# Kernel tuning notes

Hardware: AMD Instinct MI355X
Metric: run time of the kernel (lower is better)

Reference implementation:

```python
import jax, jax.numpy as jnp
import numpy as np

# Dimensions
B = 256        # number of graphs
NPG = 128      # nodes per graph (max_nodes; uniform -> to_dense_batch == reshape)
H = 8          # num_heads
DH = 32        # head_dim
HID = H * DH   # hidden_dim = 256
E = 524288     # n_edges
NGT = 20       # num_gate_types
EF = 8         # edge_feat_dim


def setup_inputs() -> dict:
    key = jax.random.key(0)
    ks = jax.random.split(key, 20)
    n_nodes = B * NPG
    x = jax.random.normal(ks[0], (n_nodes, HID), jnp.float32)
    # edges stay within the source node's graph
    src = jax.random.randint(ks[1], (E,), 0, n_nodes, dtype=jnp.int32)
    dst = (src // NPG) * NPG + jax.random.randint(ks[2], (E,), 0, NPG, dtype=jnp.int32)
    edge_index = jnp.stack([src, dst])  # [2, E]
    edge_attr = jax.random.normal(ks[3], (E, EF), jnp.float32)
    edge_gate_type = jax.random.randint(ks[4], (E,), 0, NGT, dtype=jnp.int32)
    batch = (jnp.arange(n_nodes) // NPG).astype(jnp.int32)

    s = 1.0 / np.sqrt(HID)
    def lin(k, din, dout, scale):
        kw, kb = jax.random.split(k)
        return (jax.random.uniform(kw, (din, dout), jnp.float32, -scale, scale),
                jax.random.uniform(kb, (dout,), jnp.float32, -scale, scale))
    Wq, bq = lin(ks[5], HID, HID, s)
    Wk, bk = lin(ks[6], HID, HID, s)
    Wv, bv = lin(ks[7], HID, HID, s)
    Wo, bo = lin(ks[8], HID, HID, s)
    gate_table = jax.random.normal(ks[9], (NGT, H), jnp.float32)
    We, be = lin(ks[10], EF, H, 1.0 / np.sqrt(EF))
    return {"x": x, "edge_attr": edge_attr, "Wq": Wq, "bq": bq, "Wk": Wk, "bk": bk,
            "Wv": Wv, "bv": bv, "Wo": Wo, "bo": bo, "gate_table": gate_table,
            "We": We, "be": be, "edge_index": edge_index,
            "edge_gate_type": edge_gate_type, "batch": batch}


def _edge_bias(edge_index, edge_attr, edge_gate_type, batch, gate_table, We, be):
    src, dst = edge_index[0], edge_index[1]
    eb = batch[src]                       # edge -> graph id
    src_l = src - eb * NPG                # local node index within graph
    dst_l = dst - eb * NPG
    total = gate_table[edge_gate_type] + edge_attr @ We + be   # [E, H]
    bias = jnp.zeros((B, H, NPG, NPG), edge_attr.dtype)
    bias = bias.at[eb, :, src_l, dst_l].add(total)             # forward direction
    rev = jnp.where((src_l != dst_l)[:, None], total, 0.0)     # skip self-loops
    bias = bias.at[eb, :, dst_l, src_l].add(rev)               # reverse direction
    return bias


def reference(x, edge_attr, Wq, bq, Wk, bk, Wv, bv, Wo, bo, gate_table, We, be,
              edge_index, edge_gate_type, batch):
    scale = 1.0 / np.sqrt(DH)
    xd = x.reshape(B, NPG, HID)  # uniform graph sizes -> to_dense_batch is a reshape
    Q = (xd @ Wq + bq).reshape(B, NPG, H, DH).transpose(0, 2, 1, 3)  # [B,H,N,D]
    K = (xd @ Wk + bk).reshape(B, NPG, H, DH).transpose(0, 2, 1, 3)
    V = (xd @ Wv + bv).reshape(B, NPG, H, DH).transpose(0, 2, 1, 3)
    scores = jnp.einsum('bhqd,bhkd->bhqk', Q, K) * scale
    scores = scores + _edge_bias(edge_index, edge_attr, edge_gate_type, batch,
                                 gate_table, We, be)
    attn = jax.nn.softmax(scores, axis=-1)  # node_mask all-True (uniform sizes)
    out = jnp.einsum('bhqk,bhkd->bhqd', attn, V)
    out = out.transpose(0, 2, 1, 3).reshape(B * NPG, HID)
    return out @ Wo + bo
```

## Files before the change

### kernel.cpp

```cpp
#include <hip/hip_runtime.h>
#include <hip/hip_fp16.h>

typedef unsigned short u16;
typedef unsigned int u32;
typedef __attribute__((ext_vector_type(8))) short short8;
typedef __attribute__((ext_vector_type(4))) float f32x4;

#define MFMA16(a, b, c) __builtin_amdgcn_mfma_f32_16x16x32_bf16((a), (b), (c), 0, 0, 0)

#define ESTRIDE 2304

#define FIXSCALE 16777216.0f
#define FIXINV   5.9604644775390625e-8f

__device__ __forceinline__ float b2f(u16 u) {
  union { float f; unsigned int i; } v;
  v.i = ((unsigned int)u) << 16;
  return v.f;
}
__device__ __forceinline__ u16 f2b(float f) {
  union { float f; unsigned int i; } v;
  v.f = f;
  unsigned int x = v.i;
  return (u16)((x + 0x7FFFu + ((x >> 16) & 1u)) >> 16);
}
__device__ __forceinline__ u16 f2h_bits(float f) {
  __half h = __float2half(f);
  u16 b;
  __builtin_memcpy(&b, &h, 2);
  return b;
}
__device__ __forceinline__ float h2f_bits(u16 b) {
  __half h;
  __builtin_memcpy(&h, &b, 2);
  return __half2float(h);
}

__device__ __forceinline__ void gload_lds16(const u16* g, u16* l) {
  __builtin_amdgcn_global_load_lds(
      (const __attribute__((address_space(1))) void*)g,
      (__attribute__((address_space(3))) void*)l, 16, 0, 0);
}

__global__ __launch_bounds__(256) void cvt_wtrans_kernel(
    const float* __restrict__ x, u16* __restrict__ xb,
    const float* __restrict__ W0, const float* __restrict__ W1,
    const float* __restrict__ W2, const float* __restrict__ W3,
    u16* __restrict__ T0, u16* __restrict__ T1,
    u16* __restrict__ T2, u16* __restrict__ T3) {
  int bx = blockIdx.x;
  if (bx < 4096) {
    size_t i = ((size_t)bx * 256 + threadIdx.x) * 8;
    const float4* p = (const float4*)(x + i);
    float4 v0 = p[0], v1 = p[1];
    float vf[8] = {v0.x, v0.y, v0.z, v0.w, v1.x, v1.y, v1.z, v1.w};
    short8 s;
#pragma unroll
    for (int j = 0; j < 8; ++j) s[j] = (short)f2b(vf[j]);
    *(short8*)(xb + i) = s;
  } else {
    int r = bx - 4096;
    const float* W; u16* T;
    switch (r >> 5) {
      case 0: W = W0; T = T0; break;
      case 1: W = W1; T = T1; break;
      case 2: W = W2; T = T2; break;
      default: W = W3; T = T3; break;
    }
    int n = threadIdx.x;
    int k0 = (r & 31) * 8;
    short8 s;
#pragma unroll
    for (int j = 0; j < 8; ++j) s[j] = (short)f2b(W[(size_t)(k0 + j) * 256 + n]);
    *(short8*)(T + (size_t)n * 256 + k0) = s;
  }
}

__global__ __launch_bounds__(256) void edge_build_kernel(
    const int* __restrict__ ei, const float* __restrict__ ea,
    const int* __restrict__ egt, const float* __restrict__ gate_table,
    const float* __restrict__ We, const float* __restrict__ be,
    u32* __restrict__ gfill, u16* __restrict__ etot16,
    u32* __restrict__ epos, int E) {
  __shared__ u32 hist[256];
  __shared__ u32 cursor[256];
  const int tid = threadIdx.x;
  hist[tid] = 0;
  __syncthreads();
  const int base_e = blockIdx.x * 2048;
  int gcache[8];
#pragma unroll
  for (int i = 0; i < 8; ++i) {
    int e = base_e + i * 256 + tid;
    int g = (e < E) ? (ei[e] >> 7) : -1;
    gcache[i] = g;
    if (g >= 0) atomicAdd(&hist[(u32)g], 1u);
  }
  __syncthreads();
  {
    u32 c = hist[tid];
    u32 r = c ? atomicAdd(&gfill[tid * 16], c) : 0u;
    cursor[tid] = (u32)tid * ESTRIDE + r;
  }
  __syncthreads();
#pragma unroll
  for (int i = 0; i < 8; ++i) {
    int g = gcache[i];
    if (g < 0) continue;
    int e = base_e + i * 256 + tid;
    int src = ei[e], dst = ei[E + e];
    int sl = src & 127, dl = dst & 127;
    int gt = egt[e];
    const float4* eap = (const float4*)(ea + (size_t)e * 8);
    float4 e0 = eap[0], e1 = eap[1];
    float eaf[8] = {e0.x, e0.y, e0.z, e0.w, e1.x, e1.y, e1.z, e1.w};
    short8 sv;
#pragma unroll
    for (int h = 0; h < 8; ++h) {
      float s = gate_table[gt * 8 + h] + be[h];
#pragma unroll
      for (int f = 0; f < 8; ++f) s += eaf[f] * We[f * 8 + h];
      sv[h] = (short)f2h_bits(s);
    }
    u32 pos = atomicAdd(&cursor[(u32)g], 1u);
    epos[pos] = (u32)sl | ((u32)dl << 16);
    *(short8*)(etot16 + (size_t)pos * 8) = sv;
  }
}

__global__ __launch_bounds__(256) void etrans_pad_kernel(
    const u16* __restrict__ aos, const u32* __restrict__ gfill,
    u16* __restrict__ soa, u32* __restrict__ epos) {
  int g = blockIdx.y;
  int p = blockIdx.x * 256 + threadIdx.x;
  u32 cnt = gfill[g * 16];
  size_t idx = (size_t)g * ESTRIDE + p;
  const size_t plane = (size_t)256 * ESTRIDE;
  if ((u32)p < cnt) {
    short8 v = *(const short8*)(aos + idx * 8);
#pragma unroll
    for (int h = 0; h < 8; ++h) soa[plane * h + idx] = (u16)v[h];
  } else {
    epos[idx] = 0;
#pragma unroll
    for (int h = 0; h < 8; ++h) soa[plane * h + idx] = 0;
  }
}

template <int NMAT, typename COUT>
__global__ __launch_bounds__(256) void gemm_tiled_kernel(
    const u16* __restrict__ A,
    const u16* __restrict__ T0, const u16* __restrict__ T1,
    const u16* __restrict__ T2,
    const float* __restrict__ b0, const float* __restrict__ b1,
    const float* __restrict__ b2,
    float s0, float s1, float s2,
    COUT* __restrict__ C0, COUT* __restrict__ C1, COUT* __restrict__ C2) {
  __shared__ __align__(16) u16 lA[128 * 64];
  __shared__ __align__(16) u16 lB[128 * 64];

  const int tid = threadIdx.x;
  const int bm = blockIdx.x;
  const int bn = blockIdx.y;
  const int m  = (NMAT == 1) ? 0 : (bn >> 1);
  const int ch = (NMAT == 1) ? bn : (bn & 1);

  const u16* Ts[3] = {T0, T1, T2};
  const float* bs[3] = {b0, b1, b2};
  const float scs[3] = {s0, s1, s2};
  COUT* Cs[3] = {C0, C1, C2};

  const u16* Abase = A + (size_t)(bm * 128) * 256;
  const u16* Bbase = Ts[m] + (size_t)(ch * 128) * 256;

  int srow[4];
  int selem[4];
#pragma unroll
  for (int i = 0; i < 4; ++i) {
    int c = i * 256 + tid;
    int row = c >> 3;
    int q = (c & 7) * 16;
    srow[i] = row;
    selem[i] = (q ^ ((row & 7) << 4)) >> 1;
  }

  const int wid = tid >> 6, lane = tid & 63;
  const int wm = wid >> 1, wn = wid & 1;
  const int quad = lane >> 4, l16 = lane & 15;
  const int swz = (l16 & 7) << 4;

  f32x4 acc[4][4] = {};

#pragma unroll
  for (int kt = 0; kt < 4; ++kt) {
    const int k0 = kt * 64;
    __syncthreads();
#pragma unroll
    for (int i = 0; i < 4; ++i) {
      gload_lds16(Abase + (size_t)srow[i] * 256 + k0 + selem[i],
                  lA + (size_t)(i * 256 + tid) * 8);
      gload_lds16(Bbase + (size_t)srow[i] * 256 + k0 + selem[i],
                  lB + (size_t)(i * 256 + tid) * 8);
    }
    __syncthreads();

#pragma unroll
    for (int ks = 0; ks < 2; ++ks) {
      const int kb = (ks * 64 + quad * 16) ^ swz;
      short8 af[4], bf[4];
#pragma unroll
      for (int i = 0; i < 4; ++i) {
        int arow = wm * 64 + i * 16 + l16;
        af[i] = *(const short8*)((const char*)lA + arow * 128 + kb);
        int brow = wn * 64 + i * 16 + l16;
        bf[i] = *(const short8*)((const char*)lB + brow * 128 + kb);
      }
#pragma unroll
      for (int i = 0; i < 4; ++i)
#pragma unroll
        for (int j = 0; j < 4; ++j)
          acc[i][j] = MFMA16(af[i], bf[j], acc[i][j]);
    }
  }

  const float* bias = bs[m];
  const float sc = scs[m];
  COUT* C = Cs[m];
#pragma unroll
  for (int j = 0; j < 4; ++j) {
    int col = ch * 128 + wn * 64 + j * 16 + l16;
    float bv = bias[col];
#pragma unroll
    for (int i = 0; i < 4; ++i) {
      int row0 = bm * 128 + wm * 64 + i * 16 + quad * 4;
#pragma unroll
      for (int r = 0; r < 4; ++r) {
        float o = (acc[i][j][r] + bv) * sc;
        if constexpr (sizeof(COUT) == 4)
          C[(size_t)(row0 + r) * 256 + col] = o;
        else
          C[(size_t)(row0 + r) * 256 + col] = f2b(o);
      }
    }
  }
}

__global__ __launch_bounds__(512) void attn_kernel(
    const u16* __restrict__ Q, const u16* __restrict__ K,
    const u16* __restrict__ V, const u32* __restrict__ epos,
    const u16* __restrict__ etot16, u16* __restrict__ O) {
  constexpr int LV = 144, LP = 136, LS = 132;
  __shared__ __align__(16) char smem[67584];
  int*   Si  = (int*)smem;
  u32*   Su  = (u32*)smem;
  u16*   Pb  = (u16*)smem;
  u16*   Vt  = (u16*)(smem + 34816);
  float* inv = (float*)(smem + 44032);

  const int tid = threadIdx.x;
  const int h = blockIdx.x, b = blockIdx.y;
  const int wid = tid >> 6, lane = tid & 63;
  const int quad = lane >> 4, l16 = lane & 15;

  u32 pd[5]; u16 tb[5];
  {
    const u32* ep = epos + (size_t)b * ESTRIDE + tid;
    const u16* ets = etot16 + (size_t)h * (256 * ESTRIDE) + (size_t)b * ESTRIDE + tid;
#pragma unroll
    for (int i = 0; i < 4; ++i) pd[i] = ep[i * 512];
#pragma unroll
    for (int i = 0; i < 4; ++i) tb[i] = ets[i * 512];
    if (tid < 256) { pd[4] = ep[2048]; tb[4] = ets[2048]; }
  }

  const int vr = tid >> 2, vs = (tid & 3) * 8;
  short8 vreg = *(const short8*)(V + (size_t)(b * 128 + vr) * 256 + h * 32 + vs);

  {
    short8 aq = *(const short8*)(
        Q + (size_t)(b * 128 + wid * 16 + l16) * 256 + h * 32 + quad * 8);
#pragma unroll
    for (int j = 0; j < 8; ++j) {
      short8 bk = *(const short8*)(
          K + (size_t)(b * 128 + j * 16 + l16) * 256 + h * 32 + quad * 8);
      f32x4 z = {0.f, 0.f, 0.f, 0.f};
      f32x4 sv = MFMA16(aq, bk, z);
      const int cswz = (j >> 1) << 3;
#pragma unroll
      for (int r = 0; r < 4; ++r)
        Si[(wid * 16 + quad * 4 + r) * LS + ((j * 16 + l16) ^ cswz)] =
            __float2int_rn(sv[r] * FIXSCALE);
    }
  }
  __syncthreads();

#pragma unroll
  for (int i = 0; i < 5; ++i) {
    if ((i < 4 || tid < 256) && ((pd[i] | (u32)tb[i]) != 0)) {
      int sl = pd[i] & 0xffff, dl = pd[i] >> 16;
      u32 ti = (u32)__float2int_rn(h2f_bits(tb[i]) * FIXSCALE);
      int dls = dl ^ ((dl & 0x60) >> 2);
      int sls = sl ^ ((sl & 0x60) >> 2);
      atomicAdd(&Su[sl * LS + dls], ti);
      if (sl != dl) atomicAdd(&Su[dl * LS + sls], ti);
    }
  }
  __syncthreads();

  {
    int row = tid >> 2, t4 = tid & 3, c0 = t4 * 32;
    const int* srow = &Si[row * LS];
    float sv[32];
#pragma unroll
    for (int k = 0; k < 8; ++k) {
      int4 v = *(const int4*)(srow + ((c0 + k * 4) ^ (t4 << 3)));
      sv[k * 4 + 0] = (float)v.x * FIXINV;
      sv[k * 4 + 1] = (float)v.y * FIXINV;
      sv[k * 4 + 2] = (float)v.z * FIXINV;
      sv[k * 4 + 3] = (float)v.w * FIXINV;
    }
    float m = -1e30f;
#pragma unroll
    for (int c = 0; c < 32; ++c) m = fmaxf(m, sv[c]);
    m = fmaxf(m, __shfl_xor(m, 1, 64));
    m = fmaxf(m, __shfl_xor(m, 2, 64));
    float sum = 0.f;
    short8 prow[4];
#pragma unroll
    for (int c = 0; c < 32; ++c) {
      float p = __expf(sv[c] - m);
      sum += p;
      prow[c >> 3][c & 7] = (short)f2b(p);
    }
    sum += __shfl_xor(sum, 1, 64);
    sum += __shfl_xor(sum, 2, 64);
    __syncthreads();
#pragma unroll
    for (int k = 0; k < 4; ++k)
      *(short8*)&Pb[row * LP + c0 + k * 8] = prow[k];
#pragma unroll
    for (int j = 0; j < 8; ++j)
      Vt[(vs + j) * LV + vr] = (u16)vreg[j];
    if (t4 == 0) inv[row] = 1.f / sum;
  }
  __syncthreads();

  f32x4 oacc[2] = {};
#pragma unroll
  for (int ks = 0; ks < 4; ++ks) {
    short8 ap = *(short8*)&Pb[(wid * 16 + l16) * LP + ks * 32 + quad * 8];
#pragma unroll
    for (int j = 0; j < 2; ++j) {
      short8 bv = *(short8*)&Vt[(j * 16 + l16) * LV + ks * 32 + quad * 8];
      oacc[j] = MFMA16(ap, bv, oacc[j]);
    }
  }
#pragma unroll
  for (int j = 0; j < 2; ++j)
#pragma unroll
    for (int r = 0; r < 4; ++r) {
      int qr = wid * 16 + quad * 4 + r;
      float iv = inv[qr];
      O[(size_t)(b * 128 + qr) * 256 + h * 32 + j * 16 + l16] =
          f2b(oacc[j][r] * iv);
    }
}


extern "C" void kernel_launch(void* const* d_in, const int* in_sizes, int n_in,
                              void* d_out, int out_size, void* d_ws, size_t ws_size,
                              hipStream_t stream) {
  const float* x    = (const float*)d_in[0];
  const float* ea   = (const float*)d_in[1];
  const float* Wq   = (const float*)d_in[2];
  const float* bq   = (const float*)d_in[3];
  const float* Wk   = (const float*)d_in[4];
  const float* bk   = (const float*)d_in[5];
  const float* Wv   = (const float*)d_in[6];
  const float* bv   = (const float*)d_in[7];
  const float* Wo   = (const float*)d_in[8];
  const float* bo   = (const float*)d_in[9];
  const float* gate = (const float*)d_in[10];
  const float* We   = (const float*)d_in[11];
  const float* be   = (const float*)d_in[12];
  const int*   ei   = (const int*)d_in[13];
  const int*   egt  = (const int*)d_in[14];
  const int    E    = in_sizes[14];

  const size_t matBytes = (size_t)32768 * 256 * 2;
  const size_t slots = (size_t)256 * ESTRIDE;

  char* ws = (char*)d_ws;
  u16* Qm = (u16*)ws;
  u16* Km = (u16*)(ws + matBytes);
  u16* Vm = (u16*)(ws + 2 * matBytes);
  u16* Om = (u16*)(ws + 3 * matBytes);
  u16* xb = Om;
  u16*   etA  = (u16*)(ws + 4 * matBytes);
  u16*   etS  = etA + slots * 8;
  u32*   epos = (u32*)(etS + slots * 8);
  u32*   gfill = (u32*)((char*)epos + slots * 4);
  u16*   Wtq = (u16*)((char*)gfill + 4096 * 4);
  u16*   Wtk = Wtq + 65536;
  u16*   Wtv = Wtk + 65536;
  u16*   Wto = Wtv + 65536;

  hipMemsetAsync(gfill, 0, 4096 * sizeof(u32), stream);

  edge_build_kernel<<<dim3((E + 2047) / 2048), dim3(256), 0, stream>>>(
      ei, ea, egt, gate, We, be, gfill, etA, epos, E);
  etrans_pad_kernel<<<dim3(ESTRIDE / 256, 256), dim3(256), 0, stream>>>(
      etA, gfill, etS, epos);

  cvt_wtrans_kernel<<<dim3(4224), dim3(256), 0, stream>>>(
      x, xb, Wq, Wk, Wv, Wo, Wtq, Wtk, Wtv, Wto);

  const float qscale = 0.17677669529663687f;
  gemm_tiled_kernel<3, u16><<<dim3(256, 6), dim3(256), 0, stream>>>(
      xb, Wtq, Wtk, Wtv, bq, bk, bv, qscale, 1.f, 1.f, Qm, Km, Vm);

  attn_kernel<<<dim3(8, 256), dim3(512), 0, stream>>>(
      Qm, Km, Vm, epos, etS, Om);

  gemm_tiled_kernel<1, float><<<dim3(256, 2), dim3(256), 0, stream>>>(
      Om, Wto, nullptr, nullptr, bo, nullptr, nullptr, 1.f, 1.f, 1.f,
      (float*)d_out, nullptr, nullptr);
}
```

Measured before the change: 218.6 us.

## Drop edge SoA transpose pass; read AoS edge data and count directly in attention

Removes the etrans_pad kernel that transposed per-edge bias data from AoS to per-head SoA and zero-padded unused slots. The attention kernel now reads the AoS buffer with a stride of 8 halves and uses each graph's fill count to skip dead slots instead of relying on zeroed padding. The gfill memset is folded into the conversion kernel as extra blocks. This saves a full read and write of the edge buffers and one launch, at the cost of strided, less coalesced 2-byte loads in the attention kernel.

```diff
diff --git a/kernel.cpp b/kernel.cpp
--- a/kernel.cpp
+++ b/kernel.cpp
@@ -47,7 +47,8 @@
     const float* __restrict__ W0, const float* __restrict__ W1,
     const float* __restrict__ W2, const float* __restrict__ W3,
     u16* __restrict__ T0, u16* __restrict__ T1,
-    u16* __restrict__ T2, u16* __restrict__ T3) {
+    u16* __restrict__ T2, u16* __restrict__ T3,
+    u32* __restrict__ gfill) {
   int bx = blockIdx.x;
   if (bx < 4096) {
     size_t i = ((size_t)bx * 256 + threadIdx.x) * 8;
@@ -58,7 +59,7 @@
 #pragma unroll
     for (int j = 0; j < 8; ++j) s[j] = (short)f2b(vf[j]);
     *(short8*)(xb + i) = s;
-  } else {
+  } else if (bx < 4224) {
     int r = bx - 4096;
     const float* W; u16* T;
     switch (r >> 5) {
@@ -73,6 +74,9 @@
 #pragma unroll
     for (int j = 0; j < 8; ++j) s[j] = (short)f2b(W[(size_t)(k0 + j) * 256 + n]);
     *(short8*)(T + (size_t)n * 256 + k0) = s;
+  } else {
+    int idx = (bx - 4224) * 256 + threadIdx.x;
+    gfill[idx] = 0;
   }
 }
 
@@ -128,25 +132,6 @@
   }
 }
 
-__global__ __launch_bounds__(256) void etrans_pad_kernel(
-    const u16* __restrict__ aos, const u32* __restrict__ gfill,
-    u16* __restrict__ soa, u32* __restrict__ epos) {
-  int g = blockIdx.y;
-  int p = blockIdx.x * 256 + threadIdx.x;
-  u32 cnt = gfill[g * 16];
-  size_t idx = (size_t)g * ESTRIDE + p;
-  const size_t plane = (size_t)256 * ESTRIDE;
-  if ((u32)p < cnt) {
-    short8 v = *(const short8*)(aos + idx * 8);
-#pragma unroll
-    for (int h = 0; h < 8; ++h) soa[plane * h + idx] = (u16)v[h];
-  } else {
-    epos[idx] = 0;
-#pragma unroll
-    for (int h = 0; h < 8; ++h) soa[plane * h + idx] = 0;
-  }
-}
-
 template <int NMAT, typename COUT>
 __global__ __launch_bounds__(256) void gemm_tiled_kernel(
     const u16* __restrict__ A,
@@ -248,7 +233,8 @@
 __global__ __launch_bounds__(512) void attn_kernel(
     const u16* __restrict__ Q, const u16* __restrict__ K,
     const u16* __restrict__ V, const u32* __restrict__ epos,
-    const u16* __restrict__ etot16, u16* __restrict__ O) {
+    const u16* __restrict__ etot16, const u32* __restrict__ gfill,
+    u16* __restrict__ O) {
   constexpr int LV = 144, LP = 136, LS = 132;
   __shared__ __align__(16) char smem[67584];
   int*   Si  = (int*)smem;
@@ -262,15 +248,16 @@
   const int wid = tid >> 6, lane = tid & 63;
   const int quad = lane >> 4, l16 = lane & 15;
 
+  const u32 cnt = gfill[b * 16];
   u32 pd[5]; u16 tb[5];
   {
-    const u32* ep = epos + (size_t)b * ESTRIDE + tid;
-    const u16* ets = etot16 + (size_t)h * (256 * ESTRIDE) + (size_t)b * ESTRIDE + tid;
-#pragma unroll
-    for (int i = 0; i < 4; ++i) pd[i] = ep[i * 512];
-#pragma unroll
-    for (int i = 0; i < 4; ++i) tb[i] = ets[i * 512];
-    if (tid < 256) { pd[4] = ep[2048]; tb[4] = ets[2048]; }
+    const u32* ep = epos + (size_t)b * ESTRIDE;
+    const u16* ets = etot16 + ((size_t)b * ESTRIDE) * 8 + h;
+#pragma unroll
+    for (int i = 0; i < 4; ++i) pd[i] = ep[tid + i * 512];
+#pragma unroll
+    for (int i = 0; i < 4; ++i) tb[i] = ets[(size_t)(tid + i * 512) * 8];
+    if (tid < 256) { pd[4] = ep[2048 + tid]; tb[4] = ets[(size_t)(2048 + tid) * 8]; }
   }
 
   const int vr = tid >> 2, vs = (tid & 3) * 8;
@@ -296,7 +283,9 @@
 
 #pragma unroll
   for (int i = 0; i < 5; ++i) {
-    if ((i < 4 || tid < 256) && ((pd[i] | (u32)tb[i]) != 0)) {
+    u32 slot = (i < 4) ? (u32)(tid + i * 512) : (u32)(2048 + tid);
+    bool live = (i < 4 || tid < 256) && (slot < cnt);
+    if (live) {
       int sl = pd[i] & 0xffff, dl = pd[i] >> 16;
       u32 ti = (u32)__float2int_rn(h2f_bits(tb[i]) * FIXSCALE);
       int dls = dl ^ ((dl & 0x60) >> 2);
@@ -397,30 +386,25 @@
   u16* Om = (u16*)(ws + 3 * matBytes);
   u16* xb = Om;
   u16*   etA  = (u16*)(ws + 4 * matBytes);
-  u16*   etS  = etA + slots * 8;
-  u32*   epos = (u32*)(etS + slots * 8);
+  u32*   epos = (u32*)(etA + slots * 8);
   u32*   gfill = (u32*)((char*)epos + slots * 4);
   u16*   Wtq = (u16*)((char*)gfill + 4096 * 4);
   u16*   Wtk = Wtq + 65536;
   u16*   Wtv = Wtk + 65536;
   u16*   Wto = Wtv + 65536;
 
-  hipMemsetAsync(gfill, 0, 4096 * sizeof(u32), stream);
+  cvt_wtrans_kernel<<<dim3(4240), dim3(256), 0, stream>>>(
+      x, xb, Wq, Wk, Wv, Wo, Wtq, Wtk, Wtv, Wto, gfill);
 
   edge_build_kernel<<<dim3((E + 2047) / 2048), dim3(256), 0, stream>>>(
       ei, ea, egt, gate, We, be, gfill, etA, epos, E);
-  etrans_pad_kernel<<<dim3(ESTRIDE / 256, 256), dim3(256), 0, stream>>>(
-      etA, gfill, etS, epos);
-
-  cvt_wtrans_kernel<<<dim3(4224), dim3(256), 0, stream>>>(
-      x, xb, Wq, Wk, Wv, Wo, Wtq, Wtk, Wtv, Wto);
 
   const float qscale = 0.17677669529663687f;
   gemm_tiled_kernel<3, u16><<<dim3(256, 6), dim3(256), 0, stream>>>(
       xb, Wtq, Wtk, Wtv, bq, bk, bv, qscale, 1.f, 1.f, Qm, Km, Vm);
 
   attn_kernel<<<dim3(8, 256), dim3(512), 0, stream>>>(
-      Qm, Km, Vm, epos, etS, Om);
+      Qm, Km, Vm, epos, etA, gfill, Om);
 
   gemm_tiled_kernel<1, float><<<dim3(256, 2), dim3(256), 0, stream>>>(
       Om, Wto, nullptr, nullptr, bo, nullptr, nullptr, 1.f, 1.f, 1.f,
```

Measured after the change: 221.3 us. No clear change (+1.2%).

## Keep softmax probabilities in registers as MFMA operands and fold memset into convert kernel

Applied to the files above, without the earlier changes.

Attention softmax now assigns each lane the row and column slice it will feed to the MFMA A operand. Probabilities are packed into registers instead of written to and re-read from LDS, and the max is taken on fixed-point integers. The gfill zeroing memset is merged into the conversion kernel, which now launches first, and attn gets a launch_bounds occupancy hint. This removes an LDS round trip and one launch but may raise register pressure.

```diff
diff --git a/kernel.cpp b/kernel.cpp
--- a/kernel.cpp
+++ b/kernel.cpp
@@ -35,6 +35,9 @@
   __builtin_memcpy(&h, &b, 2);
   return __half2float(h);
 }
+__device__ __forceinline__ u32 pk_bf16(float a, float b) {
+  return (u32)f2b(a) | ((u32)f2b(b) << 16);
+}
 
 __device__ __forceinline__ void gload_lds16(const u16* g, u16* l) {
   __builtin_amdgcn_global_load_lds(
@@ -47,7 +50,8 @@
     const float* __restrict__ W0, const float* __restrict__ W1,
     const float* __restrict__ W2, const float* __restrict__ W3,
     u16* __restrict__ T0, u16* __restrict__ T1,
-    u16* __restrict__ T2, u16* __restrict__ T3) {
+    u16* __restrict__ T2, u16* __restrict__ T3,
+    u32* __restrict__ gfill) {
   int bx = blockIdx.x;
   if (bx < 4096) {
     size_t i = ((size_t)bx * 256 + threadIdx.x) * 8;
@@ -58,7 +62,7 @@
 #pragma unroll
     for (int j = 0; j < 8; ++j) s[j] = (short)f2b(vf[j]);
     *(short8*)(xb + i) = s;
-  } else {
+  } else if (bx < 4224) {
     int r = bx - 4096;
     const float* W; u16* T;
     switch (r >> 5) {
@@ -73,6 +77,9 @@
 #pragma unroll
     for (int j = 0; j < 8; ++j) s[j] = (short)f2b(W[(size_t)(k0 + j) * 256 + n]);
     *(short8*)(T + (size_t)n * 256 + k0) = s;
+  } else {
+    int idx = (bx - 4224) * 256 + threadIdx.x;
+    gfill[idx] = 0;
   }
 }
 
@@ -245,15 +252,14 @@
   }
 }
 
-__global__ __launch_bounds__(512) void attn_kernel(
+__global__ __launch_bounds__(512, 4) void attn_kernel(
     const u16* __restrict__ Q, const u16* __restrict__ K,
     const u16* __restrict__ V, const u32* __restrict__ epos,
     const u16* __restrict__ etot16, u16* __restrict__ O) {
-  constexpr int LV = 144, LP = 136, LS = 132;
+  constexpr int LV = 144, LS = 132;
   __shared__ __align__(16) char smem[67584];
   int*   Si  = (int*)smem;
   u32*   Su  = (u32*)smem;
-  u16*   Pb  = (u16*)smem;
   u16*   Vt  = (u16*)(smem + 34816);
   float* inv = (float*)(smem + 44032);
 
@@ -307,52 +313,54 @@
   }
   __syncthreads();
 
+  u32 pw[16];
   {
-    int row = tid >> 2, t4 = tid & 3, c0 = t4 * 32;
+    const int row = wid * 16 + l16;
     const int* srow = &Si[row * LS];
-    float sv[32];
-#pragma unroll
-    for (int k = 0; k < 8; ++k) {
-      int4 v = *(const int4*)(srow + ((c0 + k * 4) ^ (t4 << 3)));
-      sv[k * 4 + 0] = (float)v.x * FIXINV;
-      sv[k * 4 + 1] = (float)v.y * FIXINV;
-      sv[k * 4 + 2] = (float)v.z * FIXINV;
-      sv[k * 4 + 3] = (float)v.w * FIXINV;
-    }
-    float m = -1e30f;
-#pragma unroll
-    for (int c = 0; c < 32; ++c) m = fmaxf(m, sv[c]);
-    m = fmaxf(m, __shfl_xor(m, 1, 64));
-    m = fmaxf(m, __shfl_xor(m, 2, 64));
+    int sv[32];
+#pragma unroll
+    for (int k = 0; k < 4; ++k) {
+      int cbase = 32 * k + 8 * (quad ^ k);
+      int4 v0 = *(const int4*)(srow + cbase);
+      int4 v1 = *(const int4*)(srow + cbase + 4);
+      sv[k * 8 + 0] = v0.x; sv[k * 8 + 1] = v0.y;
+      sv[k * 8 + 2] = v0.z; sv[k * 8 + 3] = v0.w;
+      sv[k * 8 + 4] = v1.x; sv[k * 8 + 5] = v1.y;
+      sv[k * 8 + 6] = v1.z; sv[k * 8 + 7] = v1.w;
+    }
+    int m = sv[0];
+#pragma unroll
+    for (int c = 1; c < 32; ++c) m = (sv[c] > m) ? sv[c] : m;
+    m = max(m, __shfl_xor(m, 16, 64));
+    m = max(m, __shfl_xor(m, 32, 64));
     float sum = 0.f;
-    short8 prow[4];
-#pragma unroll
-    for (int c = 0; c < 32; ++c) {
-      float p = __expf(sv[c] - m);
-      sum += p;
-      prow[c >> 3][c & 7] = (short)f2b(p);
-    }
-    sum += __shfl_xor(sum, 1, 64);
-    sum += __shfl_xor(sum, 2, 64);
+#pragma unroll
+    for (int w = 0; w < 16; ++w) {
+      float p0 = __expf((float)(sv[2 * w + 0] - m) * FIXINV);
+      float p1 = __expf((float)(sv[2 * w + 1] - m) * FIXINV);
+      sum += p0 + p1;
+      pw[w] = pk_bf16(p0, p1);
+    }
+    sum += __shfl_xor(sum, 16, 64);
+    sum += __shfl_xor(sum, 32, 64);
     __syncthreads();
-#pragma unroll
-    for (int k = 0; k < 4; ++k)
-      *(short8*)&Pb[row * LP + c0 + k * 8] = prow[k];
 #pragma unroll
     for (int j = 0; j < 8; ++j)
       Vt[(vs + j) * LV + vr] = (u16)vreg[j];
-    if (t4 == 0) inv[row] = 1.f / sum;
+    if (quad == 0) inv[row] = 1.f / sum;
   }
   __syncthreads();
 
   f32x4 oacc[2] = {};
 #pragma unroll
   for (int ks = 0; ks < 4; ++ks) {
-    short8 ap = *(short8*)&Pb[(wid * 16 + l16) * LP + ks * 32 + quad * 8];
+    union { u32 w[4]; short8 s; } ap;
+#pragma unroll
+    for (int j = 0; j < 4; ++j) ap.w[j] = pw[ks * 4 + j];
 #pragma unroll
     for (int j = 0; j < 2; ++j) {
       short8 bv = *(short8*)&Vt[(j * 16 + l16) * LV + ks * 32 + quad * 8];
-      oacc[j] = MFMA16(ap, bv, oacc[j]);
+      oacc[j] = MFMA16(ap.s, bv, oacc[j]);
     }
   }
 #pragma unroll
@@ -405,15 +413,14 @@
   u16*   Wtv = Wtk + 65536;
   u16*   Wto = Wtv + 65536;
 
-  hipMemsetAsync(gfill, 0, 4096 * sizeof(u32), stream);
+  cvt_wtrans_kernel<<<dim3(4240), dim3(256), 0, stream>>>(
+      x, xb, Wq, Wk, Wv, Wo, Wtq, Wtk, Wtv, Wto, gfill);
 
   edge_build_kernel<<<dim3((E + 2047) / 2048), dim3(256), 0, stream>>>(
       ei, ea, egt, gate, We, be, gfill, etA, epos, E);
+
   etrans_pad_kernel<<<dim3(ESTRIDE / 256, 256), dim3(256), 0, stream>>>(
       etA, gfill, etS, epos);
-
-  cvt_wtrans_kernel<<<dim3(4224), dim3(256), 0, stream>>>(
-      x, xb, Wq, Wk, Wv, Wo, Wtq, Wtk, Wtv, Wto);
 
   const float qscale = 0.17677669529663687f;
   gemm_tiled_kernel<3, u16><<<dim3(256, 6), dim3(256), 0, stream>>>(
```

Measured after the change: 220.4 us (median of 2 runs). No clear change (+0.8%).
